# Kernel tuning notes

Measured on AMD Instinct MI355X. Metric: run time of the kernel, lower is better.

The kernel has to match this reference:

```python
import jax, jax.numpy as jnp
import numpy as np

# Single LSTM cell step from ZERO initial state (h0=c0=0), vectorized over (B,T).
# PyTorch gate order: i, f, g, o. Since h0=0 the W_hh contribution is exactly 0
# and since c0=0 the forget-gate term vanishes: c = sigmoid(i)*tanh(g).

def _cell(inp, W_ih, b_ih, b_hh):
    # inp: (B,T,in), W_ih: (4H,in) -> gates (B,T,4H)
    g = jnp.einsum('bti,gi->btg', inp, W_ih) + b_ih + b_hh
    i_, f_, g_, o_ = jnp.split(g, 4, axis=-1)
    c = jax.nn.sigmoid(i_) * jnp.tanh(g_)
    h = jax.nn.sigmoid(o_) * jnp.tanh(c)
    return h, c


def setup_inputs() -> dict:
    key = jax.random.key(0)
    ks = jax.random.split(key, 11)
    B, T, E, H, V = 32, 256, 512, 512, 50000
    s = 1.0 / np.sqrt(H)  # keep gates out of deep saturation
    return {
        'x': jax.random.randint(ks[0], (B, T), 0, V, dtype=jnp.int32),
        'emb': jax.random.normal(ks[1], (V, E), jnp.float32),
        'W_ih_l0': jax.random.normal(ks[2], (2, 4 * H, E), jnp.float32) * s,
        'W_hh_l0': jax.random.normal(ks[3], (2, 4 * H, H), jnp.float32) * s,
        'b_ih_l0': jax.random.normal(ks[4], (2, 4 * H), jnp.float32) * s,
        'b_hh_l0': jax.random.normal(ks[5], (2, 4 * H), jnp.float32) * s,
        'W_ih_l1': jax.random.normal(ks[6], (2, 4 * H, 2 * H), jnp.float32) * s,
        'W_hh_l1': jax.random.normal(ks[7], (2, 4 * H, H), jnp.float32) * s,
        'b_ih_l1': jax.random.normal(ks[8], (2, 4 * H), jnp.float32) * s,
        'b_hh_l1': jax.random.normal(ks[9], (2, 4 * H), jnp.float32) * s,
    }


def reference(x, emb, W_ih_l0, W_hh_l0, b_ih_l0, b_hh_l0,
              W_ih_l1, W_hh_l1, b_ih_l1, b_hh_l1):
    e = emb[x]  # (B,T,E)
    # layer 0, forward/backward directions (seq_len==1 per step, so both
    # directions see the same token from zero state, with separate weights)
    h0f, c0f = _cell(e, W_ih_l0[0], b_ih_l0[0], b_hh_l0[0])
    h0b, c0b = _cell(e, W_ih_l0[1], b_ih_l0[1], b_hh_l0[1])
    inp1 = jnp.concatenate([h0f, h0b], axis=-1)  # (B,T,2H)
    h1f, c1f = _cell(inp1, W_ih_l1[0], b_ih_l1[0], b_hh_l1[0])
    h1b, c1b = _cell(inp1, W_ih_l1[1], b_ih_l1[1], b_hh_l1[1])
    # encoder_out: per-timestep h_n summed over directions -> (B,T,L,H)
    encoder_out = jnp.stack([h0f + h0b, h1f + h1b], axis=2)
    # h_last: forward-direction h_n and c_n at last timestep -> (L,B,H)
    h_last = jnp.stack([h0f[:, -1], h1f[:, -1]], axis=0)
    c_last = jnp.stack([c0f[:, -1], c1f[:, -1]], axis=0)
    return h_last, c_last, encoder_out
```

## Files before the change

kernel.cpp:

```cpp
#include <hip/hip_runtime.h>
#include <hip/hip_bf16.h>


using bf16x8 = __attribute__((ext_vector_type(8))) short;
using f32x4  = __attribute__((ext_vector_type(4))) float;

__device__ __forceinline__ float sigf(float x) { return 1.0f / (1.0f + expf(-x)); }
__device__ __forceinline__ unsigned short f2bf(float f)
{
    __hip_bfloat16 h = __float2bfloat16(f);
    return *(unsigned short*)&h;
}

__device__ __forceinline__ void gload16(const void* g, void* l)
{
    __builtin_amdgcn_global_load_lds(
        (const __attribute__((address_space(1))) unsigned int*)g,
        (__attribute__((address_space(3))) unsigned int*)l, 16, 0, 0);
}

__global__ void detect(const unsigned int* __restrict__ emb, int* __restrict__ flag)
{
    int ok = 0;
    for (int i = threadIdx.x; i < 256; i += 64) {
        unsigned lo = emb[i] & 0xFFFFu;
        int e = (lo >> 7) & 0xFF;
        if ((e >= 96 && e < 160) || lo == 0) ok++;
    }
#pragma unroll
    for (int off = 32; off; off >>= 1) ok += __shfl_down(ok, off);
    if (threadIdx.x == 0) *flag = (ok >= 192) ? 1 : 0;
}

__global__ void gather_convert(const int* __restrict__ x, const void* __restrict__ emb,
                               uint4* __restrict__ e0, const int* __restrict__ flag)
{
    int idx = blockIdx.x * 256 + threadIdx.x;
    int m = idx >> 6, r = idx & 63;
    long srow = x[m];
    uint4 v;
    if (*flag) {
        v = ((const uint4*)emb)[srow * 64 + r];
    } else {
        const float4* ef = (const float4*)emb;
        float4 a = ef[srow * 128 + r * 2], b = ef[srow * 128 + r * 2 + 1];
        unsigned short h[8] = { f2bf(a.x), f2bf(a.y), f2bf(a.z), f2bf(a.w),
                                f2bf(b.x), f2bf(b.y), f2bf(b.z), f2bf(b.w) };
        v = *(uint4*)h;
    }
    e0[idx] = v;
}

__global__ void pack_w(const void* __restrict__ src, uint4* __restrict__ dst,
                       int k8shift, const int* __restrict__ flag)
{
    int idx = blockIdx.x * 256 + threadIdx.x;
    int n = idx >> k8shift;
    int r = idx & ((1 << k8shift) - 1);
    int h = n / 6, gi = n % 6;
    int dir = (gi >= 3) ? 1 : 0;
    int gate = gi - dir * 3;
    int sg = (gate == 0) ? 0 : (gate + 1);
    long srcrow = dir * 2048 + sg * 512 + h;
    long c8 = (srcrow << k8shift) + r;
    if (*flag) {
        dst[idx] = ((const uint4*)src)[c8];
    } else {
        const float4* sf = (const float4*)src;
        float4 a = sf[c8 * 2], b = sf[c8 * 2 + 1];
        unsigned short h8[8] = { f2bf(a.x), f2bf(a.y), f2bf(a.z), f2bf(a.w),
                                 f2bf(b.x), f2bf(b.y), f2bf(b.z), f2bf(b.w) };
        dst[idx] = *(uint4*)h8;
    }
}

__global__ void pack_bias(const void* __restrict__ bi, const void* __restrict__ bh,
                          float* __restrict__ bc, const int* __restrict__ flag)
{
    int n = blockIdx.x * 256 + threadIdx.x;
    int h = n / 6, gi = n % 6;
    int dir = (gi >= 3) ? 1 : 0;
    int gate = gi - dir * 3;
    int sg = (gate == 0) ? 0 : (gate + 1);
    int s = dir * 2048 + sg * 512 + h;
    float vi, vh;
    if (*flag) {
        vi = __bfloat162float(((const __hip_bfloat16*)bi)[s]);
        vh = __bfloat162float(((const __hip_bfloat16*)bh)[s]);
    } else {
        vi = ((const float*)bi)[s];
        vh = ((const float*)bh)[s];
    }
    bc[n] = vi + vh;
}

template <int LAYER>
__global__ __launch_bounds__(256)
void gemm_fused(const unsigned short* __restrict__ A,
                const unsigned short* __restrict__ Bp,
                const float* __restrict__ bc,
                unsigned short* __restrict__ inp1,
                void* __restrict__ outv,
                const int* __restrict__ flag,
                int K)
{
    constexpr int BM = 128, BN = 96, BK = 32;
    __shared__ __align__(16) char smem[64 * 97 * 4];
    unsigned short* As = (unsigned short*)smem;
    unsigned short* Bs = (unsigned short*)(smem + 8192);
    float* Cs = (float*)smem;

    const int tid = threadIdx.x;
    const int bm = blockIdx.x;
    const int bn = blockIdx.y;
    const int K8 = K >> 3;

    const uint4* a4 = (const uint4*)A;
    const uint4* b4 = (const uint4*)Bp;
    uint4* As4 = (uint4*)As;
    uint4* Bs4 = (uint4*)Bs;

    const int ciA1 = tid + 256;
    const int ciB1 = tid + 256;
    const long aOff0 = (long)(bm * BM + (tid  >> 2)) * K8 + (tid  & 3);
    const long aOff1 = (long)(bm * BM + (ciA1 >> 2)) * K8 + (ciA1 & 3);
    const long bOff0 = (long)(bn * BN + (tid  >> 2)) * K8 + (tid  & 3);
    const long bOff1 = (long)(bn * BN + (ciB1 >> 2)) * K8 + (ciB1 & 3);

    const int wave = tid >> 6, lane = tid & 63;
    const int wr = (wave >> 1) << 6;
    const int wc = (wave & 1) * 48;
    const int lr = lane & 15, q = lane >> 4;

    f32x4 acc[4][3] = {};

    for (int k0 = 0; k0 < K; k0 += BK) {
        const int k8 = k0 >> 3;
        __syncthreads();
        gload16(a4 + aOff0 + k8, As4 + tid);
        gload16(a4 + aOff1 + k8, As4 + ciA1);
        gload16(b4 + bOff0 + k8, Bs4 + tid);
        if (tid < 128) gload16(b4 + bOff1 + k8, Bs4 + ciB1);
        __syncthreads();

        bf16x8 af[4], bf[3];
#pragma unroll
        for (int i = 0; i < 4; ++i)
            af[i] = *(const bf16x8*)&As[(wr + i * 16 + lr) * BK + q * 8];
#pragma unroll
        for (int j = 0; j < 3; ++j)
            bf[j] = *(const bf16x8*)&Bs[(wc + j * 16 + lr) * BK + q * 8];
#pragma unroll
        for (int i = 0; i < 4; ++i)
#pragma unroll
            for (int j = 0; j < 3; ++j)
                acc[i][j] = __builtin_amdgcn_mfma_f32_16x16x32_bf16(af[i], bf[j], acc[i][j], 0, 0, 0);
    }

    const bool isbf = (*flag != 0);
    auto store = [&](long i, float v) {
        if (isbf) ((__hip_bfloat16*)outv)[i] = __float2bfloat16(v);
        else      ((float*)outv)[i] = v;
    };

    const int hl = tid & 15;
    float bcv[6];
#pragma unroll
    for (int gi = 0; gi < 6; ++gi) bcv[gi] = bc[bn * BN + hl * 6 + gi];

#pragma unroll
    for (int pass = 0; pass < 2; ++pass) {
        __syncthreads();
        if ((wr >> 6) == pass) {
#pragma unroll
            for (int i = 0; i < 4; ++i)
#pragma unroll
                for (int j = 0; j < 3; ++j)
#pragma unroll
                    for (int r = 0; r < 4; ++r)
                        Cs[(i * 16 + q * 4 + r) * 97 + wc + j * 16 + lr] = acc[i][j][r];
        }
        __syncthreads();
#pragma unroll
        for (int t = 0; t < 4; ++t) {
            int ml = (tid >> 4) + t * 16;
            float z[6];
#pragma unroll
            for (int gi = 0; gi < 6; ++gi) z[gi] = Cs[ml * 97 + hl * 6 + gi] + bcv[gi];
            float c0 = sigf(z[0]) * tanhf(z[1]);
            float h0 = sigf(z[2]) * tanhf(c0);
            float c1 = sigf(z[3]) * tanhf(z[4]);
            float h1 = sigf(z[5]) * tanhf(c1);

            long m = (long)bm * BM + pass * 64 + ml;
            int hg = bn * 16 + hl;

            if constexpr (LAYER == 0) {
                inp1[m * 1024 + hg]       = f2bf(h0);
                inp1[m * 1024 + 512 + hg] = f2bf(h1);
            }
            store(65536 + m * 1024 + LAYER * 512 + hg, h0 + h1);
            if ((m & 255) == 255) {
                int b = (int)(m >> 8);
                store(LAYER * 16384 + b * 512 + hg, h0);
                store(32768 + LAYER * 16384 + b * 512 + hg, c0);
            }
        }
    }
}

extern "C" void kernel_launch(void* const* d_in, const int* in_sizes, int n_in,
                              void* d_out, int out_size, void* d_ws, size_t ws_size,
                              hipStream_t stream)
{
    const int* x      = (const int*)d_in[0];
    const void* emb   = d_in[1];
    const void* Wih0  = d_in[2];
    const void* bih0  = d_in[4];
    const void* bhh0  = d_in[5];
    const void* Wih1  = d_in[6];
    const void* bih1  = d_in[8];
    const void* bhh1  = d_in[9];

    char* ws = (char*)d_ws;
    int*   flag           = (int*)(ws);
    float* bc0            = (float*)(ws + 1024);
    float* bc1            = (float*)(ws + 16384);
    unsigned short* Wp0   = (unsigned short*)(ws + 32768);
    unsigned short* Wp1   = (unsigned short*)(ws + 4194304);
    unsigned short* e0    = (unsigned short*)(ws + 10485760);
    unsigned short* inp1  = (unsigned short*)(ws + 18874368);

    detect<<<1, 64, 0, stream>>>((const unsigned int*)emb, flag);
    gather_convert<<<2048, 256, 0, stream>>>(x, emb, (uint4*)e0, flag);
    pack_w<<<768, 256, 0, stream>>>(Wih0, (uint4*)Wp0, 6, flag);
    pack_w<<<1536, 256, 0, stream>>>(Wih1, (uint4*)Wp1, 7, flag);
    pack_bias<<<12, 256, 0, stream>>>(bih0, bhh0, bc0, flag);
    pack_bias<<<12, 256, 0, stream>>>(bih1, bhh1, bc1, flag);

    gemm_fused<0><<<dim3(64, 32), 256, 0, stream>>>(e0, Wp0, bc0, inp1, d_out, flag, 512);
    gemm_fused<1><<<dim3(64, 32), 256, 0, stream>>>(inp1, Wp1, bc1, nullptr, d_out, flag, 1024);
}
```

Measured before the change: 314.5 us.

## Fuse prep kernels, double-buffer GEMM loads, enlarge tiles, use fast transcendentals

Merges the detect, gather, weight-pack and bias-pack kernels into one prep launch, where each block re-derives the dtype flag locally. The GEMM moves to 512-thread blocks with BM=256 and double-buffers the A/B LDS stages, so the next tile's global loads overlap the current MFMAs with one barrier per iteration. The epilogue uses __expf-based sigmoid and tanh instead of expf/tanhf. These target launch overhead, load latency and epilogue cost, at the price of more LDS per block, fewer blocks in the grid and slightly less accurate activations.

```diff
diff --git a/kernel.cpp b/kernel.cpp
--- a/kernel.cpp
+++ b/kernel.cpp
@@ -5,11 +5,15 @@
 using bf16x8 = __attribute__((ext_vector_type(8))) short;
 using f32x4  = __attribute__((ext_vector_type(4))) float;
 
-__device__ __forceinline__ float sigf(float x) { return 1.0f / (1.0f + expf(-x)); }
 __device__ __forceinline__ unsigned short f2bf(float f)
 {
     __hip_bfloat16 h = __float2bfloat16(f);
     return *(unsigned short*)&h;
+}
+__device__ __forceinline__ float sigf(float x)  { return 1.0f / (1.0f + __expf(-x)); }
+__device__ __forceinline__ float tanhfast(float x)
+{
+    return 1.0f - 2.0f / (__expf(2.0f * x) + 1.0f);
 }
 
 __device__ __forceinline__ void gload16(const void* g, void* l)
@@ -19,83 +23,90 @@
         (__attribute__((address_space(3))) unsigned int*)l, 16, 0, 0);
 }
 
-__global__ void detect(const unsigned int* __restrict__ emb, int* __restrict__ flag)
-{
-    int ok = 0;
-    for (int i = threadIdx.x; i < 256; i += 64) {
-        unsigned lo = emb[i] & 0xFFFFu;
+__global__ __launch_bounds__(256)
+void prep(const int* __restrict__ x, const void* __restrict__ emb,
+          const void* __restrict__ Wih0, const void* __restrict__ Wih1,
+          const void* __restrict__ bih0, const void* __restrict__ bhh0,
+          const void* __restrict__ bih1, const void* __restrict__ bhh1,
+          uint4* __restrict__ e0, uint4* __restrict__ Wp0, uint4* __restrict__ Wp1,
+          float* __restrict__ bc0, float* __restrict__ bc1, int* __restrict__ flag)
+{
+    __shared__ int oks[4];
+    {
+        unsigned lo = ((const unsigned int*)emb)[threadIdx.x] & 0xFFFFu;
         int e = (lo >> 7) & 0xFF;
-        if ((e >= 96 && e < 160) || lo == 0) ok++;
-    }
-#pragma unroll
-    for (int off = 32; off; off >>= 1) ok += __shfl_down(ok, off);
-    if (threadIdx.x == 0) *flag = (ok >= 192) ? 1 : 0;
-}
-
-__global__ void gather_convert(const int* __restrict__ x, const void* __restrict__ emb,
-                               uint4* __restrict__ e0, const int* __restrict__ flag)
-{
-    int idx = blockIdx.x * 256 + threadIdx.x;
-    int m = idx >> 6, r = idx & 63;
-    long srow = x[m];
-    uint4 v;
-    if (*flag) {
-        v = ((const uint4*)emb)[srow * 64 + r];
+        int ok = ((e >= 96 && e < 160) || lo == 0) ? 1 : 0;
+#pragma unroll
+        for (int off = 32; off; off >>= 1) ok += __shfl_down(ok, off);
+        if ((threadIdx.x & 63) == 0) oks[threadIdx.x >> 6] = ok;
+    }
+    __syncthreads();
+    const bool isbf = (oks[0] + oks[1] + oks[2] + oks[3]) >= 192;
+    const int bid = blockIdx.x, tid = threadIdx.x;
+
+    if (bid < 2048) {
+        int idx = bid * 256 + tid;
+        int m = idx >> 6, r = idx & 63;
+        long srow = x[m];
+        uint4 v;
+        if (isbf) {
+            v = ((const uint4*)emb)[srow * 64 + r];
+        } else {
+            const float4* ef = (const float4*)emb;
+            float4 a = ef[srow * 128 + r * 2], b = ef[srow * 128 + r * 2 + 1];
+            unsigned short h[8] = { f2bf(a.x), f2bf(a.y), f2bf(a.z), f2bf(a.w),
+                                    f2bf(b.x), f2bf(b.y), f2bf(b.z), f2bf(b.w) };
+            v = *(uint4*)h;
+        }
+        e0[idx] = v;
+    } else if (bid < 4352) {
+        const bool L0 = bid < 2816;
+        const int  ks = L0 ? 6 : 7;
+        int idx = (L0 ? (bid - 2048) : (bid - 2816)) * 256 + tid;
+        const void* src = L0 ? Wih0 : Wih1;
+        uint4* dst = L0 ? Wp0 : Wp1;
+        int n = idx >> ks, r = idx & ((1 << ks) - 1);
+        int h = n / 6, gi = n % 6;
+        int dir = (gi >= 3) ? 1 : 0;
+        int gate = gi - dir * 3;
+        int sg = (gate == 0) ? 0 : (gate + 1);
+        long c8 = ((long)(dir * 2048 + sg * 512 + h) << ks) + r;
+        if (isbf) {
+            dst[idx] = ((const uint4*)src)[c8];
+        } else {
+            const float4* sf = (const float4*)src;
+            float4 a = sf[c8 * 2], b = sf[c8 * 2 + 1];
+            unsigned short h8[8] = { f2bf(a.x), f2bf(a.y), f2bf(a.z), f2bf(a.w),
+                                     f2bf(b.x), f2bf(b.y), f2bf(b.z), f2bf(b.w) };
+            dst[idx] = *(uint4*)h8;
+        }
     } else {
-        const float4* ef = (const float4*)emb;
-        float4 a = ef[srow * 128 + r * 2], b = ef[srow * 128 + r * 2 + 1];
-        unsigned short h[8] = { f2bf(a.x), f2bf(a.y), f2bf(a.z), f2bf(a.w),
-                                f2bf(b.x), f2bf(b.y), f2bf(b.z), f2bf(b.w) };
-        v = *(uint4*)h;
-    }
-    e0[idx] = v;
-}
-
-__global__ void pack_w(const void* __restrict__ src, uint4* __restrict__ dst,
-                       int k8shift, const int* __restrict__ flag)
-{
-    int idx = blockIdx.x * 256 + threadIdx.x;
-    int n = idx >> k8shift;
-    int r = idx & ((1 << k8shift) - 1);
-    int h = n / 6, gi = n % 6;
-    int dir = (gi >= 3) ? 1 : 0;
-    int gate = gi - dir * 3;
-    int sg = (gate == 0) ? 0 : (gate + 1);
-    long srcrow = dir * 2048 + sg * 512 + h;
-    long c8 = (srcrow << k8shift) + r;
-    if (*flag) {
-        dst[idx] = ((const uint4*)src)[c8];
-    } else {
-        const float4* sf = (const float4*)src;
-        float4 a = sf[c8 * 2], b = sf[c8 * 2 + 1];
-        unsigned short h8[8] = { f2bf(a.x), f2bf(a.y), f2bf(a.z), f2bf(a.w),
-                                 f2bf(b.x), f2bf(b.y), f2bf(b.z), f2bf(b.w) };
-        dst[idx] = *(uint4*)h8;
-    }
-}
-
-__global__ void pack_bias(const void* __restrict__ bi, const void* __restrict__ bh,
-                          float* __restrict__ bc, const int* __restrict__ flag)
-{
-    int n = blockIdx.x * 256 + threadIdx.x;
-    int h = n / 6, gi = n % 6;
-    int dir = (gi >= 3) ? 1 : 0;
-    int gate = gi - dir * 3;
-    int sg = (gate == 0) ? 0 : (gate + 1);
-    int s = dir * 2048 + sg * 512 + h;
-    float vi, vh;
-    if (*flag) {
-        vi = __bfloat162float(((const __hip_bfloat16*)bi)[s]);
-        vh = __bfloat162float(((const __hip_bfloat16*)bh)[s]);
-    } else {
-        vi = ((const float*)bi)[s];
-        vh = ((const float*)bh)[s];
-    }
-    bc[n] = vi + vh;
+        int b2 = bid - 4352;
+        if (b2 == 0 && tid == 0) *flag = isbf ? 1 : 0;
+        const bool L0 = b2 < 12;
+        int n = (L0 ? b2 : (b2 - 12)) * 256 + tid;
+        int h = n / 6, gi = n % 6;
+        int dir = (gi >= 3) ? 1 : 0;
+        int gate = gi - dir * 3;
+        int sg = (gate == 0) ? 0 : (gate + 1);
+        int s = dir * 2048 + sg * 512 + h;
+        const void* bi = L0 ? bih0 : bih1;
+        const void* bh = L0 ? bhh0 : bhh1;
+        float* bc = L0 ? bc0 : bc1;
+        float vi, vh;
+        if (isbf) {
+            vi = __bfloat162float(((const __hip_bfloat16*)bi)[s]);
+            vh = __bfloat162float(((const __hip_bfloat16*)bh)[s]);
+        } else {
+            vi = ((const float*)bi)[s];
+            vh = ((const float*)bh)[s];
+        }
+        bc[n] = vi + vh;
+    }
 }
 
 template <int LAYER>
-__global__ __launch_bounds__(256)
+__global__ __launch_bounds__(512)
 void gemm_fused(const unsigned short* __restrict__ A,
                 const unsigned short* __restrict__ Bp,
                 const float* __restrict__ bc,
@@ -104,45 +115,41 @@
                 const int* __restrict__ flag,
                 int K)
 {
-    constexpr int BM = 128, BN = 96, BK = 32;
-    __shared__ __align__(16) char smem[64 * 97 * 4];
-    unsigned short* As = (unsigned short*)smem;
-    unsigned short* Bs = (unsigned short*)(smem + 8192);
-    float* Cs = (float*)smem;
-
-    const int tid = threadIdx.x;
-    const int bm = blockIdx.x;
-    const int bn = blockIdx.y;
+    constexpr int BM = 256, BN = 96, BK = 32;
+    __shared__ __align__(16) char smem[45056];
+
+    const int tid = threadIdx.x, bm = blockIdx.x, bn = blockIdx.y;
     const int K8 = K >> 3;
-
     const uint4* a4 = (const uint4*)A;
     const uint4* b4 = (const uint4*)Bp;
-    uint4* As4 = (uint4*)As;
-    uint4* Bs4 = (uint4*)Bs;
-
-    const int ciA1 = tid + 256;
-    const int ciB1 = tid + 256;
-    const long aOff0 = (long)(bm * BM + (tid  >> 2)) * K8 + (tid  & 3);
-    const long aOff1 = (long)(bm * BM + (ciA1 >> 2)) * K8 + (ciA1 & 3);
-    const long bOff0 = (long)(bn * BN + (tid  >> 2)) * K8 + (tid  & 3);
-    const long bOff1 = (long)(bn * BN + (ciB1 >> 2)) * K8 + (ciB1 & 3);
+
+    const long aBase0 = (long)(bm * BM + (tid >> 2)) * K8 + (tid & 3);
+    const long aBase1 = aBase0 + (long)128 * K8;
+    const long bBase0 = (long)(bn * BN + (tid >> 2)) * K8 + (tid & 3);
+    const bool bact = tid < 384;
 
     const int wave = tid >> 6, lane = tid & 63;
-    const int wr = (wave >> 1) << 6;
+    const int wr = (wave >> 1) * 64;
     const int wc = (wave & 1) * 48;
     const int lr = lane & 15, q = lane >> 4;
 
     f32x4 acc[4][3] = {};
-
-    for (int k0 = 0; k0 < K; k0 += BK) {
-        const int k8 = k0 >> 3;
-        __syncthreads();
-        gload16(a4 + aOff0 + k8, As4 + tid);
-        gload16(a4 + aOff1 + k8, As4 + ciA1);
-        gload16(b4 + bOff0 + k8, Bs4 + tid);
-        if (tid < 128) gload16(b4 + bOff1 + k8, Bs4 + ciB1);
-        __syncthreads();
-
+    const int NT = K / BK;
+
+    auto stage = [&](int buf, int k8) {
+        uint4* As4 = (uint4*)(smem + buf * 16384);
+        uint4* Bs4 = (uint4*)(smem + 32768 + buf * 6144);
+        gload16(a4 + aBase0 + k8, As4 + tid);
+        gload16(a4 + aBase1 + k8, As4 + tid + 512);
+        if (bact) gload16(b4 + bBase0 + k8, Bs4 + tid);
+    };
+
+    stage(0, 0);
+    __syncthreads();
+    for (int t = 0; t < NT; ++t) {
+        if (t + 1 < NT) stage((t + 1) & 1, (t + 1) * (BK >> 3));
+        const unsigned short* As = (const unsigned short*)(smem + (t & 1) * 16384);
+        const unsigned short* Bs = (const unsigned short*)(smem + 32768 + (t & 1) * 6144);
         bf16x8 af[4], bf[3];
 #pragma unroll
         for (int i = 0; i < 4; ++i)
@@ -155,8 +162,10 @@
 #pragma unroll
             for (int j = 0; j < 3; ++j)
                 acc[i][j] = __builtin_amdgcn_mfma_f32_16x16x32_bf16(af[i], bf[j], acc[i][j], 0, 0, 0);
-    }
-
+        __syncthreads();
+    }
+
+    float* Cs = (float*)smem;
     const bool isbf = (*flag != 0);
     auto store = [&](long i, float v) {
         if (isbf) ((__hip_bfloat16*)outv)[i] = __float2bfloat16(v);
@@ -168,10 +177,8 @@
 #pragma unroll
     for (int gi = 0; gi < 6; ++gi) bcv[gi] = bc[bn * BN + hl * 6 + gi];
 
-#pragma unroll
-    for (int pass = 0; pass < 2; ++pass) {
-        __syncthreads();
-        if ((wr >> 6) == pass) {
+    for (int p = 0; p < 4; ++p) {
+        if ((wave >> 1) == p) {
 #pragma unroll
             for (int i = 0; i < 4; ++i)
 #pragma unroll
@@ -182,17 +189,17 @@
         }
         __syncthreads();
 #pragma unroll
-        for (int t = 0; t < 4; ++t) {
-            int ml = (tid >> 4) + t * 16;
+        for (int t2 = 0; t2 < 2; ++t2) {
+            int ml = (tid >> 4) + t2 * 32;
             float z[6];
 #pragma unroll
             for (int gi = 0; gi < 6; ++gi) z[gi] = Cs[ml * 97 + hl * 6 + gi] + bcv[gi];
-            float c0 = sigf(z[0]) * tanhf(z[1]);
-            float h0 = sigf(z[2]) * tanhf(c0);
-            float c1 = sigf(z[3]) * tanhf(z[4]);
-            float h1 = sigf(z[5]) * tanhf(c1);
-
-            long m = (long)bm * BM + pass * 64 + ml;
+            float c0 = sigf(z[0]) * tanhfast(z[1]);
+            float h0 = sigf(z[2]) * tanhfast(c0);
+            float c1 = sigf(z[3]) * tanhfast(z[4]);
+            float h1 = sigf(z[5]) * tanhfast(c1);
+
+            long m = (long)bm * BM + p * 64 + ml;
             int hg = bn * 16 + hl;
 
             if constexpr (LAYER == 0) {
@@ -206,6 +213,7 @@
                 store(32768 + LAYER * 16384 + b * 512 + hg, c0);
             }
         }
+        if (p < 3) __syncthreads();
     }
 }
 
@@ -231,13 +239,9 @@
     unsigned short* e0    = (unsigned short*)(ws + 10485760);
     unsigned short* inp1  = (unsigned short*)(ws + 18874368);
 
-    detect<<<1, 64, 0, stream>>>((const unsigned int*)emb, flag);
-    gather_convert<<<2048, 256, 0, stream>>>(x, emb, (uint4*)e0, flag);
-    pack_w<<<768, 256, 0, stream>>>(Wih0, (uint4*)Wp0, 6, flag);
-    pack_w<<<1536, 256, 0, stream>>>(Wih1, (uint4*)Wp1, 7, flag);
-    pack_bias<<<12, 256, 0, stream>>>(bih0, bhh0, bc0, flag);
-    pack_bias<<<12, 256, 0, stream>>>(bih1, bhh1, bc1, flag);
-
-    gemm_fused<0><<<dim3(64, 32), 256, 0, stream>>>(e0, Wp0, bc0, inp1, d_out, flag, 512);
-    gemm_fused<1><<<dim3(64, 32), 256, 0, stream>>>(inp1, Wp1, bc1, nullptr, d_out, flag, 1024);
-}
+    prep<<<4376, 256, 0, stream>>>(x, emb, Wih0, Wih1, bih0, bhh0, bih1, bhh1,
+                                   (uint4*)e0, (uint4*)Wp0, (uint4*)Wp1, bc0, bc1, flag);
+
+    gemm_fused<0><<<dim3(32, 32), 512, 0, stream>>>(e0, Wp0, bc0, inp1, d_out, flag, 512);
+    gemm_fused<1><<<dim3(32, 32), 512, 0, stream>>>(inp1, Wp1, bc1, nullptr, d_out, flag, 1024);
+}
```

After: 298.1 us. -5.2%, faster.
